# Optimization experiments

Hardware: AMD Instinct MI355X
Metric: run time of the kernel (lower is better)

## Reference

```python
import jax, jax.numpy as jnp
import numpy as np

B, C, H, W = 8, 512, 64, 64
WS, NH = 8, 16
HD = C // NH
SCALE = float(HD) ** -0.5
L = WS * WS  # tokens per window
BN_EPS = 1e-5


def _rel_index():
    # Swin relative position index, (L, L) int table into (2*WS-1)^2 bias rows
    ch = np.arange(WS)
    coords = np.stack(np.meshgrid(ch, ch, indexing='ij'))  # (2, WS, WS)
    cf = coords.reshape(2, -1)
    rel = cf[:, :, None] - cf[:, None, :]
    rel = rel.transpose(1, 2, 0).copy()
    rel[:, :, 0] += WS - 1
    rel[:, :, 1] += WS - 1
    rel[:, :, 0] *= 2 * WS - 1
    return jnp.asarray(rel.sum(-1))

REL_IDX = _rel_index()


def conv2d(x, w, pad=0, groups=1):
    return jax.lax.conv_general_dilated(
        x, w, (1, 1), [(pad, pad), (pad, pad)],
        feature_group_count=groups,
        dimension_numbers=('NCHW', 'OIHW', 'NCHW'))


def bn(x, g, b):
    # eval-mode BatchNorm with running_mean=0, running_var=1 (fresh init)
    inv = 1.0 / np.sqrt(1.0 + BN_EPS)
    return g[None, :, None, None] * (x * inv) + b[None, :, None, None]


def avgpool(x, kh, kw, ph, pw):
    # torch AvgPool2d: zero padding, count_include_pad=True
    s = jax.lax.reduce_window(x, 0.0, jax.lax.add, (1, 1, kh, kw), (1, 1, 1, 1),
                              ((0, 0), (0, 0), (ph, ph), (pw, pw)))
    return s / (kh * kw)


def setup_inputs() -> dict:
    key = jax.random.key(0)
    ks = jax.random.split(key, 8)
    r = lambda k, s: jax.random.normal(k, s, dtype=jnp.float32) * 0.02
    return {
        'x': jax.random.normal(ks[0], (B, C, H, W), dtype=jnp.float32),
        'w_lc1': r(ks[1], (C, C, 1, 1)),
        'g1': jnp.ones((C,), jnp.float32), 'b1': jnp.zeros((C,), jnp.float32),
        'w_lc2': r(ks[2], (C, C, 3, 3)),
        'g2': jnp.ones((C,), jnp.float32), 'b2': jnp.zeros((C,), jnp.float32),
        'w_qkv': r(ks[3], (3 * C, C, 1, 1)),
        'rel_table': r(ks[4], ((2 * WS - 1) * (2 * WS - 1), NH)),
        'w_dw': r(ks[5], (C, 1, WS, WS)),
        'g3': jnp.ones((C,), jnp.float32), 'b3': jnp.zeros((C,), jnp.float32),
        'w_pw': r(ks[6], (C, C, 1, 1)),
    }


def reference(x, w_lc1, g1, b1, w_lc2, g2, b2, w_qkv, rel_table, w_dw, g3, b3, w_pw):
    # local branch: 1x1 conv+BN  +  3x3 conv+BN
    local = bn(conv2d(x, w_lc1), g1, b1) + bn(conv2d(x, w_lc2, pad=1), g2, b2)

    # H, W divisible by WS -> pad() is a no-op; Hp, Wp = H, W
    hh, ww = H // WS, W // WS
    qkv = conv2d(x, w_qkv)  # (B, 3C, H, W)
    # 'b (qkv h d) (hh ws1) (ww ws2) -> qkv (b hh ww) h (ws1 ws2) d'
    qkv = qkv.reshape(B, 3, NH, HD, hh, WS, ww, WS)
    qkv = qkv.transpose(1, 0, 4, 6, 2, 5, 7, 3).reshape(3, B * hh * ww, NH, L, HD)
    q, k, v = qkv[0], qkv[1], qkv[2]

    dots = jnp.einsum('bhid,bhjd->bhij', q, k) * SCALE  # (Bw, NH, L, L)
    bias = rel_table[REL_IDX]                            # (L, L, NH)
    dots = dots + bias.transpose(2, 0, 1)[None]
    attn = jax.nn.softmax(dots, axis=-1)
    out = jnp.einsum('bhij,bhjd->bhid', attn, v)         # (Bw, NH, L, HD)

    # '(b hh ww) h (ws1 ws2) d -> b (h d) (hh ws1) (ww ws2)'
    out = out.reshape(B, hh, ww, NH, WS, WS, HD)
    out = out.transpose(0, 3, 6, 1, 4, 2, 5).reshape(B, C, H, W)

    ax = avgpool(jnp.pad(out, ((0, 0), (0, 0), (0, 1), (0, 0)), mode='reflect'),
                 WS, 1, WS // 2 - 1, 0)
    ay = avgpool(jnp.pad(out, ((0, 0), (0, 0), (0, 0), (0, 1)), mode='reflect'),
                 1, WS, 0, WS // 2 - 1)
    out = ax + ay + local

    # pad_out + SeparableConvBN(kernel=WS): depthwise conv -> BN -> 1x1 conv
    out = jnp.pad(out, ((0, 0), (0, 0), (0, 1), (0, 1)), mode='reflect')
    out = conv2d(out, w_dw, pad=(WS - 1) // 2, groups=C)
    out = bn(out, g3, b3)
    out = conv2d(out, w_pw)
    return out[:, :, :H, :W]
```

## Files before the change

### kernel.cpp

```cpp
#include <hip/hip_runtime.h>

#define INVBN 0.9999950000374997f
#define ATT_SCALE 0.17677669529663687f

typedef short bf16x8 __attribute__((ext_vector_type(8)));
typedef float f32x4  __attribute__((ext_vector_type(4)));
typedef unsigned short us8v __attribute__((ext_vector_type(8)));

#define AS1C(p) ((const __attribute__((address_space(1))) void*)(p))
#define AS3(p)  ((__attribute__((address_space(3))) void*)(p))

#define VMCNT_BARRIER(Nstr) do {                                   \
    asm volatile("s_waitcnt vmcnt(" Nstr ")" ::: "memory");        \
    __builtin_amdgcn_s_barrier(); } while (0)

__device__ __forceinline__ float bf2f(unsigned short u) {
    return __uint_as_float(((unsigned)u) << 16);
}
__device__ __forceinline__ unsigned short f2bf(float f) {
    unsigned u = __float_as_uint(f);
    u += 0x7FFFu + ((u >> 16) & 1u);
    return (unsigned short)(u >> 16);
}

__global__ __launch_bounds__(256)
void repack_kernel(const float* __restrict__ W2, const float* __restrict__ W1,
                   const float* __restrict__ Wq, const float* __restrict__ Wp,
                   const float* __restrict__ g1, const float* __restrict__ g2,
                   const float* __restrict__ b1, const float* __restrict__ b2,
                   const float* __restrict__ RT,
                   unsigned short* __restrict__ Wt, unsigned short* __restrict__ WqO,
                   unsigned short* __restrict__ WpO, float* __restrict__ bsum,
                   float* __restrict__ biasM)
{
    int i = blockIdx.x * 256 + threadIdx.x;
    if (i < 512) bsum[i] = b1[i] + b2[i];
    if (i < 786432) WqO[i] = f2bf(Wq[i]);
    if (i < 262144) WpO[i] = f2bf(Wp[i]);
    if (i < 16384) {
        int h = i >> 10, rem = i & 1023;
        int frag = rem >> 6, lane = rem & 63;
        int fi = frag >> 2, fj = frag & 3;
        int q  = 16 * fj + (lane & 15);
        int kb = 16 * fi + ((lane >> 4) << 2);
        int yi = q >> 3, xi = q & 7;
        float4 o;
        float* op = (float*)&o;
#pragma unroll
        for (int r = 0; r < 4; ++r) {
            int j = kb + r;
            int ridx = (yi - (j >> 3) + 7) * 15 + (xi - (j & 7) + 7);
            op[r] = RT[ridx * 16 + h];
        }
        *(float4*)&biasM[(size_t)i * 4] = o;
    }
    if (i >= 2359296) return;
    int tap = i / 262144;
    int rem = i - tap * 262144;
    int m   = rem >> 9;
    float v = g2[m] * INVBN * W2[(size_t)rem * 9 + tap];
    if (tap == 4) v = fmaf(g1[m] * INVBN, W1[rem], v);
    Wt[i] = f2bf(v);
}

__global__ __launch_bounds__(256)
void pad_transpose_kernel(const float* __restrict__ X, unsigned short* __restrict__ XT)
{
    int ph = blockIdx.x;
    int b  = blockIdx.y;
    int t  = threadIdx.x;
    unsigned short* rowbase = XT + ((size_t)b * 4356 + (size_t)ph * 66) * 512;
    uint4 z = make_uint4(0, 0, 0, 0);
    if (ph == 0 || ph == 65) {
        uint4* p4 = (uint4*)rowbase;
        for (int i = t; i < 4224; i += 256) p4[i] = z;
        return;
    }
    if (t < 64)       ((uint4*)rowbase)[t] = z;
    else if (t < 128) ((uint4*)(rowbase + 65 * 512))[t - 64] = z;

    int h = ph - 1;
    __shared__ float tile[64][65];
    const float* xb = X + (size_t)b * 512 * 4096 + h * 64;
    for (int cc = 0; cc < 8; ++cc) {
        int c0 = cc * 64;
        __syncthreads();
#pragma unroll
        for (int i = 0; i < 4; ++i) {
            int cl = i * 16 + (t >> 4);
            int w0 = (t & 15) * 4;
            *(float4*)&tile[cl][w0] =
                *(const float4*)&xb[(size_t)(c0 + cl) * 4096 + w0];
        }
        __syncthreads();
#pragma unroll
        for (int it = 0; it < 2; ++it) {
            int wl = it * 32 + (t >> 3);
            int cs = (t & 7) * 8;
            us8v v;
#pragma unroll
            for (int e = 0; e < 8; ++e) v[e] = f2bf(tile[cs + e][wl]);
            *(us8v*)&rowbase[(size_t)(1 + wl) * 512 + c0 + cs] = v;
        }
    }
}

template<int NTAPS, bool PAD, typename OT>
__global__ __launch_bounds__(512, 2)
void mfma_gemm256(const unsigned short* __restrict__ A,
                  const unsigned short* __restrict__ Bw,
                  const float* __restrict__ bias,
                  OT* __restrict__ Out, int M)
{
    __shared__ __align__(16) unsigned short ldsbuf[65536];

    const int t    = threadIdx.x;
    const int wid  = t >> 6, lane = t & 63;
    const int wr   = wid >> 2, wc = wid & 3;
    const int lrow = lane & 15, lk = lane >> 4;
    const int n0 = blockIdx.x * 256;
    const int m0 = blockIdx.y * 256;
    const int b  = blockIdx.z;
    const unsigned short* Ab = A + (size_t)b * (PAD ? 4356 * 512 : 4096 * 512);
    OT* Ob = Out + (size_t)b * ((size_t)M * 4096);

    const unsigned short* src[4];
    {
        int rsub = lane >> 2, ch = lane & 3;
        int chs  = ch ^ ((rsub >> 1) & 3);
#pragma unroll
        for (int i = 0; i < 4; ++i) {
            if (wid < 4) {
                int p = n0 + (wid * 4 + i) * 16 + rsub;
                if (PAD) {
                    int h = p >> 6, w = p & 63;
                    src[i] = Ab + (size_t)((h + 1) * 66 + (w + 1)) * 512 + chs * 8;
                } else {
                    src[i] = Ab + (size_t)p * 512 + chs * 8;
                }
            } else {
                int m = m0 + ((wid - 4) * 4 + i) * 16 + rsub;
                src[i] = Bw + (size_t)m * 512 + chs * 8;
            }
        }
    }

    f32x4 acc[8][4] = {};

    const int ck0 = (lk ^ ((lrow >> 1) & 3)) * 8;

    auto aScal = [&](int tt) -> int {
        if (NTAPS == 1) return tt * 32;
        int tap = tt >> 4;
        return (tap / 3 - 1) * (66 * 512) + (tap % 3 - 1) * 512 + (tt & 15) * 32;
    };
    auto bScal = [&](int tt) -> int {
        if (NTAPS == 1) return tt * 32;
        return (tt >> 4) * (M * 512) + (tt & 15) * 32;
    };
    auto STAGE = [&](int bufk, int aoff, int boff) {
        int off = (wid < 4) ? aoff : boff;
#pragma unroll
        for (int i = 0; i < 4; ++i)
            __builtin_amdgcn_global_load_lds(
                AS1C(src[i] + off),
                AS3(&ldsbuf[bufk * 16384 + (wid * 4 + i) * 512]), 16, 0, 0);
    };
    auto COMPUTE = [&](int bufk) {
        const unsigned short* Ak = &ldsbuf[bufk * 16384];
        const unsigned short* Bk = &ldsbuf[bufk * 16384 + 8192];
        bf16x8 af[8], bfr[4];
#pragma unroll
        for (int f = 0; f < 8; ++f)
            af[f] = *(const bf16x8*)&Ak[(wr * 128 + f * 16 + lrow) * 32 + ck0];
#pragma unroll
        for (int g = 0; g < 4; ++g)
            bfr[g] = *(const bf16x8*)&Bk[(wc * 64 + g * 16 + lrow) * 32 + ck0];
        __builtin_amdgcn_s_setprio(1);
#pragma unroll
        for (int f = 0; f < 8; ++f)
#pragma unroll
            for (int g = 0; g < 4; ++g)
                acc[f][g] = __builtin_amdgcn_mfma_f32_16x16x32_bf16(
                    af[f], bfr[g], acc[f][g], 0, 0, 0);
        __builtin_amdgcn_s_setprio(0);
    };

    constexpr int NT = NTAPS * 16;

    STAGE(0, aScal(0), bScal(0));
    STAGE(1, aScal(1), bScal(1));
    STAGE(2, aScal(2), bScal(2));
    VMCNT_BARRIER("8");

#pragma unroll 1
    for (int tb = 0; tb < NT - 4; tb += 4) {
        STAGE(3, aScal(tb + 3), bScal(tb + 3)); COMPUTE(0); VMCNT_BARRIER("8");
        STAGE(0, aScal(tb + 4), bScal(tb + 4)); COMPUTE(1); VMCNT_BARRIER("8");
        STAGE(1, aScal(tb + 5), bScal(tb + 5)); COMPUTE(2); VMCNT_BARRIER("8");
        STAGE(2, aScal(tb + 6), bScal(tb + 6)); COMPUTE(3); VMCNT_BARRIER("8");
    }
    STAGE(3, aScal(NT - 1), bScal(NT - 1)); COMPUTE(0); VMCNT_BARRIER("8");
    COMPUTE(1); VMCNT_BARRIER("4");
    COMPUTE(2); VMCNT_BARRIER("0");
    COMPUTE(3);

#pragma unroll
    for (int g = 0; g < 4; ++g) {
        int m = m0 + wc * 64 + g * 16 + lrow;
        float bv = bias ? bias[m] : 0.f;
        size_t mrow = (size_t)m * 4096;
#pragma unroll
        for (int f = 0; f < 8; ++f) {
            int nb = n0 + wr * 128 + f * 16 + lk * 4;
            f32x4 a4 = acc[f][g];
            if constexpr (sizeof(OT) == 2) {
                ushort4 o;
                o.x = f2bf(a4[0] + bv);
                o.y = f2bf(a4[1] + bv);
                o.z = f2bf(a4[2] + bv);
                o.w = f2bf(a4[3] + bv);
                *(ushort4*)&Ob[mrow + nb] = o;
            } else {
                *(float4*)&Ob[mrow + nb] =
                    make_float4(a4[0] + bv, a4[1] + bv, a4[2] + bv, a4[3] + bv);
            }
        }
    }
}

__global__ __launch_bounds__(256)
void attn_mfma_kernel(const unsigned short* __restrict__ QKV,
                      const float* __restrict__ biasM,
                      unsigned short* __restrict__ OutB)
{
    __shared__ short smem[4 * 9216];
    int t = threadIdx.x;
    int wv = t >> 6, lane = t & 63;
    int wing = blockIdx.x >> 2;
    int head = (blockIdx.x & 3) * 4 + wv;
    int b    = blockIdx.y;
    int hhi = wing >> 3, wwi = wing & 7;
    int sp0 = hhi * 512 + wwi * 8;
    int ch0 = head * 32;
    const unsigned short* Qg = QKV + (size_t)b * 1536 * 4096;

    short* Qtm = smem + wv * 9216;
    short* Ktm = Qtm + 2304;
    short* Pq  = Qtm + 4608;

    {
        int d  = lane & 31;
        int rb = lane >> 5;
#pragma unroll
        for (int i = 0; i < 4; ++i) {
            int r = rb + 2 * i;
            us8v q8 = *(const us8v*)&Qg[(size_t)(ch0 + d) * 4096 + sp0 + r * 64];
            us8v k8 = *(const us8v*)&Qg[(size_t)(512 + ch0 + d) * 4096 + sp0 + r * 64];
#pragma unroll
            for (int e = 0; e < 8; ++e) {
                Qtm[(r * 8 + e) * 36 + d] = (short)q8[e];
                Ktm[(r * 8 + e) * 36 + d] = (short)k8[e];
            }
        }
    }

    int lrow = lane & 15, lk = lane >> 4;

    bf16x8 kf[4], qf[4];
#pragma unroll
    for (int f = 0; f < 4; ++f) {
        kf[f] = *(const bf16x8*)&Ktm[(lrow + 16 * f) * 36 + lk * 8];
        qf[f] = *(const bf16x8*)&Qtm[(lrow + 16 * f) * 36 + lk * 8];
    }
    f32x4 s[4][4] = {};
#pragma unroll
    for (int fi = 0; fi < 4; ++fi)
#pragma unroll
        for (int fj = 0; fj < 4; ++fj)
            s[fi][fj] = __builtin_amdgcn_mfma_f32_16x16x32_bf16(
                kf[fi], qf[fj], s[fi][fj], 0, 0, 0);

    const float* bM = biasM + (size_t)head * 4096;
    float rs[4];
#pragma unroll
    for (int fj = 0; fj < 4; ++fj) {
        float v[4][4];
#pragma unroll
        for (int fi = 0; fi < 4; ++fi) {
            float4 bv = *(const float4*)&bM[((fi * 4 + fj) * 64 + lane) * 4];
            const float* bvp = (const float*)&bv;
#pragma unroll
            for (int r = 0; r < 4; ++r)
                v[fi][r] = fmaf(s[fi][fj][r], ATT_SCALE, bvp[r]);
        }
        float m = -1e30f;
#pragma unroll
        for (int fi = 0; fi < 4; ++fi)
#pragma unroll
            for (int r = 0; r < 4; ++r) m = fmaxf(m, v[fi][r]);
        m = fmaxf(m, __shfl_xor(m, 16));
        m = fmaxf(m, __shfl_xor(m, 32));
        float ev[4][4];
        float sum = 0.f;
#pragma unroll
        for (int fi = 0; fi < 4; ++fi)
#pragma unroll
            for (int r = 0; r < 4; ++r) {
                ev[fi][r] = __expf(v[fi][r] - m);
                sum += ev[fi][r];
            }
        sum += __shfl_xor(sum, 16);
        sum += __shfl_xor(sum, 32);
        rs[fj] = 1.f / sum;
#pragma unroll
        for (int fi = 0; fi < 4; ++fi) {
            unsigned p0 = (unsigned)f2bf(ev[fi][0]) | ((unsigned)f2bf(ev[fi][1]) << 16);
            unsigned p1 = (unsigned)f2bf(ev[fi][2]) | ((unsigned)f2bf(ev[fi][3]) << 16);
            *(uint2*)&Pq[(lrow + 16 * fj) * 72 + 16 * fi + lk * 4] = make_uint2(p0, p1);
        }
    }

    f32x4 o[2][4] = {};
#pragma unroll
    for (int ks = 0; ks < 2; ++ks) {
        bf16x8 vf[2], pf[4];
#pragma unroll
        for (int fid = 0; fid < 2; ++fid)
            vf[fid] = *(const bf16x8*)&Qg[(size_t)(1024 + ch0 + 16 * fid + lrow) * 4096
                                          + sp0 + (lk + 4 * ks) * 64];
#pragma unroll
        for (int fjq = 0; fjq < 4; ++fjq)
            pf[fjq] = *(const bf16x8*)&Pq[(lrow + 16 * fjq) * 72 + ks * 32 + lk * 8];
#pragma unroll
        for (int fid = 0; fid < 2; ++fid)
#pragma unroll
            for (int fjq = 0; fjq < 4; ++fjq)
                o[fid][fjq] = __builtin_amdgcn_mfma_f32_16x16x32_bf16(
                    vf[fid], pf[fjq], o[fid][fjq], 0, 0, 0);
    }

#pragma unroll
    for (int fjq = 0; fjq < 4; ++fjq) {
        int q = lrow + 16 * fjq;
        float rr = rs[fjq];
#pragma unroll
        for (int fid = 0; fid < 2; ++fid) {
            int dch = 16 * fid + lk * 4;
#pragma unroll
            for (int r = 0; r < 4; ++r)
                Pq[(dch + r) * 72 + q] = (short)f2bf(o[fid][fjq][r] * rr);
        }
    }
    unsigned short* Out = OutB + (size_t)b * 512 * 4096;
#pragma unroll
    for (int j = 0; j < 4; ++j) {
        int dch  = lane & 31;
        int tokc = (lane >> 5) + 2 * j;
        us8v vv = *(const us8v*)&Pq[dch * 72 + tokc * 8];
        *(us8v*)&Out[(size_t)(ch0 + dch) * 4096 + sp0 + tokc * 64] = vv;
    }
}

__global__ __launch_bounds__(256)
void pooldw_kernel(const unsigned short* __restrict__ A, const unsigned short* __restrict__ L,
                   const float* __restrict__ Wd,
                   const float* __restrict__ g3, const float* __restrict__ b3,
                   unsigned short* __restrict__ U)
{
    int bc = blockIdx.x;
    int c  = bc & 511;
    __shared__ float pad[72][72];
    int t = threadIdx.x;
    float* pf = &pad[0][0];
#pragma unroll
    for (int i = 0; i < 21; ++i) {
        int e = i * 256 + t;
        if (e < 5184) pf[e] = 0.f;
    }
    __syncthreads();

    const unsigned short* ap = A + (size_t)bc * 4096;
#pragma unroll
    for (int i = 0; i < 4; ++i) {
        int idx = i * 256 + t;
        int y = idx >> 4, x4 = (idx & 15) * 4;
        ushort4 a4 = ((const ushort4*)ap)[idx];
        *(float4*)&pad[3 + y][4 + x4] =
            make_float4(bf2f(a4.x), bf2f(a4.y), bf2f(a4.z), bf2f(a4.w));
    }
    if (t < 64)       pad[67][4 + t] = bf2f(ap[62 * 64 + t]);
    else if (t < 128) { int y = t - 64; pad[3 + y][68] = bf2f(ap[y * 64 + 62]); }
    else if (t == 128) pad[67][68] = bf2f(ap[62 * 64 + 62]);
    __syncthreads();

    const unsigned short* lp = L + (size_t)bc * 4096;
    int u  = t & 7, rr = t >> 3;
    int w0 = u * 8;
    float res[2][8];
#pragma unroll
    for (int g = 0; g < 2; ++g) {
        int h = g * 32 + rr;
        float4 sxlo = make_float4(0.f, 0.f, 0.f, 0.f);
        float4 sxhi = make_float4(0.f, 0.f, 0.f, 0.f);
#pragma unroll
        for (int i = 0; i < 8; ++i) {
            float4 a = *(const float4*)&pad[h + i][4 + w0];
            float4 bq = *(const float4*)&pad[h + i][8 + w0];
            sxlo.x += a.x; sxlo.y += a.y; sxlo.z += a.z; sxlo.w += a.w;
            sxhi.x += bq.x; sxhi.y += bq.y; sxhi.z += bq.z; sxhi.w += bq.w;
        }
        float sx[8] = {sxlo.x, sxlo.y, sxlo.z, sxlo.w, sxhi.x, sxhi.y, sxhi.z, sxhi.w};
        float win[16];
        *(float4*)&win[0]  = *(const float4*)&pad[3 + h][w0];
        *(float4*)&win[4]  = *(const float4*)&pad[3 + h][w0 + 4];
        *(float4*)&win[8]  = *(const float4*)&pad[3 + h][w0 + 8];
        *(float4*)&win[12] = *(const float4*)&pad[3 + h][w0 + 12];
        us8v l8 = *(const us8v*)&lp[h * 64 + w0];
#pragma unroll
        for (int p = 0; p < 8; ++p) {
            float sy = 0.f;
#pragma unroll
            for (int i = 1; i <= 8; ++i) sy += win[p + i];
            res[g][p] = fmaf(0.125f, sx[p] + sy, bf2f((unsigned short)l8[p]));
        }
    }
    __syncthreads();

#pragma unroll
    for (int g = 0; g < 2; ++g) {
        int h = g * 32 + rr;
        *(float4*)&pad[3 + h][4 + w0] = make_float4(res[g][0], res[g][1], res[g][2], res[g][3]);
        *(float4*)&pad[3 + h][8 + w0] = make_float4(res[g][4], res[g][5], res[g][6], res[g][7]);
    }
    __syncthreads();
    if (t < 64)       pad[67][4 + t] = pad[65][4 + t];
    else if (t < 128) { int y = t - 64; pad[3 + y][68] = pad[3 + y][66]; }
    else if (t == 128) pad[67][68] = pad[65][66];
    __syncthreads();

    const float* wdp = Wd + c * 64;
    float gc  = g3[c] * INVBN;
    float bcv = b3[c];
#pragma unroll
    for (int g = 0; g < 2; ++g) {
        int h = g * 32 + rr;
        float acc2[8];
#pragma unroll
        for (int p = 0; p < 8; ++p) acc2[p] = 0.f;
#pragma unroll
        for (int i = 0; i < 8; ++i) {
            float win[16];
            *(float4*)&win[0]  = *(const float4*)&pad[h + i][w0];
            *(float4*)&win[4]  = *(const float4*)&pad[h + i][w0 + 4];
            *(float4*)&win[8]  = *(const float4*)&pad[h + i][w0 + 8];
            *(float4*)&win[12] = *(const float4*)&pad[h + i][w0 + 12];
#pragma unroll
            for (int j = 0; j < 8; ++j) {
                float wv = wdp[i * 8 + j];
#pragma unroll
                for (int p = 0; p < 8; ++p)
                    acc2[p] = fmaf(wv, win[p + 1 + j], acc2[p]);
            }
        }
        us8v o8;
#pragma unroll
        for (int p = 0; p < 8; ++p) o8[p] = (short)f2bf(gc * acc2[p] + bcv);
        *(us8v*)&U[(size_t)bc * 4096 + h * 64 + w0] = o8;
    }
}

__global__ __launch_bounds__(256)
void transpose_cp_kernel(const unsigned short* __restrict__ U, unsigned short* __restrict__ Ut)
{
    int pt = blockIdx.x;
    int b  = blockIdx.y;
    const unsigned short* Ub = U + (size_t)b * 512 * 4096;
    unsigned short* Utb = Ut + (size_t)b * 4096 * 512;
    __shared__ unsigned short tile[64][72];
    int t = threadIdx.x;
    int p0 = pt * 64;

    for (int cc = 0; cc < 8; ++cc) {
        int c0 = cc * 64;
        __syncthreads();
        {
            int cl = t >> 2, px = (t & 3) * 16;
            const unsigned short* src = &Ub[(size_t)(c0 + cl) * 4096 + p0 + px];
            *(us8v*)&tile[cl][px]     = *(const us8v*)src;
            *(us8v*)&tile[cl][px + 8] = *(const us8v*)(src + 8);
        }
        __syncthreads();
        {
            int pl = t >> 2, cx = (t & 3) * 16;
            us8v o0, o1;
#pragma unroll
            for (int e = 0; e < 8; ++e) {
                o0[e] = tile[cx + e][pl];
                o1[e] = tile[cx + 8 + e][pl];
            }
            unsigned short* dst = &Utb[(size_t)(p0 + pl) * 512 + c0 + cx];
            *(us8v*)dst       = o0;
            *(us8v*)(dst + 8) = o1;
        }
    }
}

extern "C" void kernel_launch(void* const* d_in, const int* in_sizes, int n_in,
                              void* d_out, int out_size, void* d_ws, size_t ws_size,
                              hipStream_t stream)
{
    (void)in_sizes; (void)n_in; (void)out_size;
    const float* x     = (const float*)d_in[0];
    const float* w_lc1 = (const float*)d_in[1];
    const float* g1    = (const float*)d_in[2];
    const float* b1    = (const float*)d_in[3];
    const float* w_lc2 = (const float*)d_in[4];
    const float* g2    = (const float*)d_in[5];
    const float* b2    = (const float*)d_in[6];
    const float* w_qkv = (const float*)d_in[7];
    const float* rt    = (const float*)d_in[8];
    const float* w_dw  = (const float*)d_in[9];
    const float* g3    = (const float*)d_in[10];
    const float* b3    = (const float*)d_in[11];
    const float* w_pw  = (const float*)d_in[12];
    float* out = (float*)d_out;

    unsigned short* S        = (unsigned short*)d_ws;
    unsigned short* local_us = S;
    unsigned short* xt_us    = S + 16777216;
    unsigned short* attnO    = xt_us;
    unsigned short* u_us     = xt_us;
    unsigned short* wt3_us   = S + 34619392;
    unsigned short* wq_us    = S + 36978688;
    unsigned short* wpw_us   = S + 37765120;
    float*          bsum     = (float*)(S + 38027264);
    float*          biasM    = (float*)(S + 38028288);
    unsigned short* qkv_us   = S + 38552576;
    unsigned short* ut_us    = local_us;

    const bool full = ws_size >= (size_t)(38552576 + 50331648) * 2;

    repack_kernel<<<dim3(9216), 256, 0, stream>>>(w_lc2, w_lc1, w_qkv, w_pw,
                                                  g1, g2, b1, b2, rt,
                                                  wt3_us, wq_us, wpw_us, bsum, biasM);
    pad_transpose_kernel<<<dim3(66, 8), 256, 0, stream>>>(x, xt_us);
    mfma_gemm256<9, true, unsigned short><<<dim3(16, 2, 8), 512, 0, stream>>>(
        xt_us, wt3_us, bsum, local_us, 512);

    if (full) {
        mfma_gemm256<1, true, unsigned short><<<dim3(16, 6, 8), 512, 0, stream>>>(
            xt_us, wq_us, nullptr, qkv_us, 1536);
        attn_mfma_kernel<<<dim3(256, 8), 256, 0, stream>>>(qkv_us, biasM, attnO);
    } else {
        for (int b = 0; b < 8; ++b) {
            mfma_gemm256<1, true, unsigned short><<<dim3(16, 6, 1), 512, 0, stream>>>(
                xt_us + (size_t)b * 4356 * 512, wq_us, nullptr, qkv_us, 1536);
            attn_mfma_kernel<<<dim3(256, 1), 256, 0, stream>>>(
                qkv_us, biasM, attnO + (size_t)b * 2097152);
        }
    }

    pooldw_kernel<<<dim3(4096), 256, 0, stream>>>(attnO, local_us, w_dw, g3, b3, u_us);
    transpose_cp_kernel<<<dim3(64, 8), 256, 0, stream>>>(u_us, ut_us);
    mfma_gemm256<1, false, float><<<dim3(16, 2, 8), 512, 0, stream>>>(
        ut_us, wpw_us, nullptr, out, 512);
}
```

Baseline: 466.3 us.

## Fuse QKV projection GEMM into window attention kernel

Replaces the separate QKV GEMM and attention kernels with one kernel. Each block stages a window's 64 tokens of transposed input into LDS, and each wave computes its head's Q, K and V with MFMA, reading weights directly from global memory. The bf16 QKV intermediate no longer makes a round trip through HBM, and the per-batch fallback path is removed. In exchange, the 64x512 input tile is re-loaded by each of the four head-group blocks per window, and unblocked weight reads from global may have poor reuse.

```diff
diff --git a/kernel.cpp b/kernel.cpp
--- a/kernel.cpp
+++ b/kernel.cpp
@@ -146,7 +146,6 @@
     }
 
     f32x4 acc[8][4] = {};
-
     const int ck0 = (lk ^ ((lrow >> 1) & 3)) * 8;
 
     auto aScal = [&](int tt) -> int {
@@ -230,42 +229,80 @@
 }
 
 __global__ __launch_bounds__(256)
-void attn_mfma_kernel(const unsigned short* __restrict__ QKV,
-                      const float* __restrict__ biasM,
-                      unsigned short* __restrict__ OutB)
-{
-    __shared__ short smem[4 * 9216];
+void fused_qkv_attn_kernel(const unsigned short* __restrict__ XT,
+                           const unsigned short* __restrict__ W,
+                           const float* __restrict__ biasM,
+                           unsigned short* __restrict__ OutB)
+{
+    __shared__ __align__(16) unsigned short xts[32768];
+    __shared__ short pws[4][6912];
+
     int t = threadIdx.x;
-    int wv = t >> 6, lane = t & 63;
-    int wing = blockIdx.x >> 2;
-    int head = (blockIdx.x & 3) * 4 + wv;
-    int b    = blockIdx.y;
+    int wid = t >> 6, lane = t & 63;
+    int wing = blockIdx.y, b = blockIdx.z;
+    int head = blockIdx.x * 4 + wid;
     int hhi = wing >> 3, wwi = wing & 7;
     int sp0 = hhi * 512 + wwi * 8;
     int ch0 = head * 32;
-    const unsigned short* Qg = QKV + (size_t)b * 1536 * 4096;
-
-    short* Qtm = smem + wv * 9216;
+    const unsigned short* xtb = XT + (size_t)b * (4356 * 512);
+
+#pragma unroll
+    for (int rd = 0; rd < 16; ++rd) {
+        int tk  = rd * 4 + wid;
+        int rr  = tk >> 3, cdx = tk & 7;
+        int grow = (hhi * 8 + rr + 1) * 66 + (wwi * 8 + cdx + 1);
+        int cs  = lane ^ (tk & 7);
+        __builtin_amdgcn_global_load_lds(
+            AS1C(xtb + (size_t)grow * 512 + cs * 8),
+            AS3(&xts[tk * 512 + lane * 8]), 16, 0, 0);
+    }
+    asm volatile("s_waitcnt vmcnt(0)" ::: "memory");
+    __builtin_amdgcn_s_barrier();
+
+    int lrow = lane & 15, lk = lane >> 4;
+    short* Qtm = pws[wid];
     short* Ktm = Qtm + 2304;
-    short* Pq  = Qtm + 4608;
-
-    {
-        int d  = lane & 31;
-        int rb = lane >> 5;
-#pragma unroll
-        for (int i = 0; i < 4; ++i) {
-            int r = rb + 2 * i;
-            us8v q8 = *(const us8v*)&Qg[(size_t)(ch0 + d) * 4096 + sp0 + r * 64];
-            us8v k8 = *(const us8v*)&Qg[(size_t)(512 + ch0 + d) * 4096 + sp0 + r * 64];
-#pragma unroll
-            for (int e = 0; e < 8; ++e) {
-                Qtm[(r * 8 + e) * 36 + d] = (short)q8[e];
-                Ktm[(r * 8 + e) * 36 + d] = (short)k8[e];
+    short* Vtm = Qtm + 4608;
+    short* Pq  = Qtm;
+
+#pragma unroll 1
+    for (int mtx = 0; mtx < 3; ++mtx) {
+        const unsigned short* wbase = W + (size_t)(mtx * 512 + ch0) * 512;
+        f32x4 aq[4][2] = {};
+#pragma unroll
+        for (int ks = 0; ks < 16; ++ks) {
+            bf16x8 b0 = *(const bf16x8*)&wbase[(size_t)lrow * 512 + ks * 32 + lk * 8];
+            bf16x8 b1 = *(const bf16x8*)&wbase[(size_t)(16 + lrow) * 512 + ks * 32 + lk * 8];
+#pragma unroll
+            for (int tf = 0; tf < 4; ++tf) {
+                int row = tf * 16 + lrow;
+                int cc  = (ks * 4 + lk) ^ (row & 7);
+                bf16x8 af = *(const bf16x8*)&xts[row * 512 + cc * 8];
+                aq[tf][0] = __builtin_amdgcn_mfma_f32_16x16x32_bf16(af, b0, aq[tf][0], 0, 0, 0);
+                aq[tf][1] = __builtin_amdgcn_mfma_f32_16x16x32_bf16(af, b1, aq[tf][1], 0, 0, 0);
             }
         }
-    }
-
-    int lrow = lane & 15, lk = lane >> 4;
+        if (mtx < 2) {
+            short* dst = (mtx == 0) ? Qtm : Ktm;
+#pragma unroll
+            for (int tf = 0; tf < 4; ++tf)
+#pragma unroll
+                for (int cf = 0; cf < 2; ++cf)
+#pragma unroll
+                    for (int r = 0; r < 4; ++r)
+                        dst[(16 * tf + lk * 4 + r) * 36 + 16 * cf + lrow] =
+                            (short)f2bf(aq[tf][cf][r]);
+        } else {
+#pragma unroll
+            for (int tf = 0; tf < 4; ++tf)
+#pragma unroll
+                for (int cf = 0; cf < 2; ++cf)
+#pragma unroll
+                    for (int r = 0; r < 4; ++r)
+                        Vtm[(16 * cf + lrow) * 72 + 16 * tf + lk * 4 + r] =
+                            (short)f2bf(aq[tf][cf][r]);
+        }
+    }
 
     bf16x8 kf[4], qf[4];
 #pragma unroll
@@ -327,8 +364,7 @@
         bf16x8 vf[2], pf[4];
 #pragma unroll
         for (int fid = 0; fid < 2; ++fid)
-            vf[fid] = *(const bf16x8*)&Qg[(size_t)(1024 + ch0 + 16 * fid + lrow) * 4096
-                                          + sp0 + (lk + 4 * ks) * 64];
+            vf[fid] = *(const bf16x8*)&Vtm[(16 * fid + lrow) * 72 + (lk + 4 * ks) * 8];
 #pragma unroll
         for (int fjq = 0; fjq < 4; ++fjq)
             pf[fjq] = *(const bf16x8*)&Pq[(lrow + 16 * fjq) * 72 + ks * 32 + lk * 8];
@@ -510,7 +546,7 @@
                               void* d_out, int out_size, void* d_ws, size_t ws_size,
                               hipStream_t stream)
 {
-    (void)in_sizes; (void)n_in; (void)out_size;
+    (void)in_sizes; (void)n_in; (void)out_size; (void)ws_size;
     const float* x     = (const float*)d_in[0];
     const float* w_lc1 = (const float*)d_in[1];
     const float* g1    = (const float*)d_in[2];
@@ -529,17 +565,14 @@
     unsigned short* S        = (unsigned short*)d_ws;
     unsigned short* local_us = S;
     unsigned short* xt_us    = S + 16777216;
-    unsigned short* attnO    = xt_us;
-    unsigned short* u_us     = xt_us;
     unsigned short* wt3_us   = S + 34619392;
     unsigned short* wq_us    = S + 36978688;
     unsigned short* wpw_us   = S + 37765120;
     float*          bsum     = (float*)(S + 38027264);
     float*          biasM    = (float*)(S + 38028288);
-    unsigned short* qkv_us   = S + 38552576;
+    unsigned short* attnO    = S + 38552576;
+    unsigned short* u_us     = attnO;
     unsigned short* ut_us    = local_us;
-
-    const bool full = ws_size >= (size_t)(38552576 + 50331648) * 2;
 
     repack_kernel<<<dim3(9216), 256, 0, stream>>>(w_lc2, w_lc1, w_qkv, w_pw,
                                                   g1, g2, b1, b2, rt,
@@ -547,20 +580,8 @@
     pad_transpose_kernel<<<dim3(66, 8), 256, 0, stream>>>(x, xt_us);
     mfma_gemm256<9, true, unsigned short><<<dim3(16, 2, 8), 512, 0, stream>>>(
         xt_us, wt3_us, bsum, local_us, 512);
-
-    if (full) {
-        mfma_gemm256<1, true, unsigned short><<<dim3(16, 6, 8), 512, 0, stream>>>(
-            xt_us, wq_us, nullptr, qkv_us, 1536);
-        attn_mfma_kernel<<<dim3(256, 8), 256, 0, stream>>>(qkv_us, biasM, attnO);
-    } else {
-        for (int b = 0; b < 8; ++b) {
-            mfma_gemm256<1, true, unsigned short><<<dim3(16, 6, 1), 512, 0, stream>>>(
-                xt_us + (size_t)b * 4356 * 512, wq_us, nullptr, qkv_us, 1536);
-            attn_mfma_kernel<<<dim3(256, 1), 256, 0, stream>>>(
-                qkv_us, biasM, attnO + (size_t)b * 2097152);
-        }
-    }
-
+    fused_qkv_attn_kernel<<<dim3(4, 64, 8), 256, 0, stream>>>(
+        xt_us, wq_us, biasM, attnO);
     pooldw_kernel<<<dim3(4096), 256, 0, stream>>>(attnO, local_us, w_dw, g3, b3, u_us);
     transpose_cp_kernel<<<dim3(64, 8), 256, 0, stream>>>(u_us, ut_us);
     mfma_gemm256<1, false, float><<<dim3(16, 2, 8), 512, 0, stream>>>(
```

New measurement: 516.9 us. +10.8%, slower.

## Switch GEMM pipeline to double-buffered BK=64 stages with one block per CU

Applied to the files above, without the earlier changes.

Replaces the 4-stage BK=32 global_load_lds ring with a 2-stage BK=64 double buffer, using an 8-chunk XOR swizzle in LDS and two k-substeps per compute. Launch bounds drop to one 512-thread block per CU. The aim is to halve the number of barriers per K and give each wave more MFMA work per stage. The cost is shallower prefetch, an extra barrier after each compute, and less latency hiding from a second resident block.

```diff
diff --git a/kernel.cpp b/kernel.cpp
--- a/kernel.cpp
+++ b/kernel.cpp
@@ -9,10 +9,6 @@
 
 #define AS1C(p) ((const __attribute__((address_space(1))) void*)(p))
 #define AS3(p)  ((__attribute__((address_space(3))) void*)(p))
-
-#define VMCNT_BARRIER(Nstr) do {                                   \
-    asm volatile("s_waitcnt vmcnt(" Nstr ")" ::: "memory");        \
-    __builtin_amdgcn_s_barrier(); } while (0)
 
 __device__ __forceinline__ float bf2f(unsigned short u) {
     return __uint_as_float(((unsigned)u) << 16);
@@ -106,7 +102,7 @@
 }
 
 template<int NTAPS, bool PAD, typename OT>
-__global__ __launch_bounds__(512, 2)
+__global__ __launch_bounds__(512, 1)
 void mfma_gemm256(const unsigned short* __restrict__ A,
                   const unsigned short* __restrict__ Bw,
                   const float* __restrict__ bias,
@@ -124,14 +120,15 @@
     const unsigned short* Ab = A + (size_t)b * (PAD ? 4356 * 512 : 4096 * 512);
     OT* Ob = Out + (size_t)b * ((size_t)M * 4096);
 
-    const unsigned short* src[4];
+    const unsigned short* src[8];
     {
-        int rsub = lane >> 2, ch = lane & 3;
-        int chs  = ch ^ ((rsub >> 1) & 3);
-#pragma unroll
-        for (int i = 0; i < 4; ++i) {
+        int rsub = lane >> 3, ch = lane & 7;
+        int chs  = ch ^ rsub;
+#pragma unroll
+        for (int i = 0; i < 8; ++i) {
+            int row = (wid & 3) * 64 + i * 8 + rsub;
             if (wid < 4) {
-                int p = n0 + (wid * 4 + i) * 16 + rsub;
+                int p = n0 + row;
                 if (PAD) {
                     int h = p >> 6, w = p & 63;
                     src[i] = Ab + (size_t)((h + 1) * 66 + (w + 1)) * 512 + chs * 8;
@@ -139,71 +136,70 @@
                     src[i] = Ab + (size_t)p * 512 + chs * 8;
                 }
             } else {
-                int m = m0 + ((wid - 4) * 4 + i) * 16 + rsub;
-                src[i] = Bw + (size_t)m * 512 + chs * 8;
+                src[i] = Bw + (size_t)(m0 + row) * 512 + chs * 8;
             }
         }
     }
+    const int dbase = (wid >> 2) * 16384 + (wid & 3) * 4096;
 
     f32x4 acc[8][4] = {};
 
-    const int ck0 = (lk ^ ((lrow >> 1) & 3)) * 8;
-
     auto aScal = [&](int tt) -> int {
-        if (NTAPS == 1) return tt * 32;
-        int tap = tt >> 4;
-        return (tap / 3 - 1) * (66 * 512) + (tap % 3 - 1) * 512 + (tt & 15) * 32;
+        if (NTAPS == 1) return tt * 64;
+        int tap = tt >> 3;
+        return (tap / 3 - 1) * (66 * 512) + (tap % 3 - 1) * 512 + (tt & 7) * 64;
     };
     auto bScal = [&](int tt) -> int {
-        if (NTAPS == 1) return tt * 32;
-        return (tt >> 4) * (M * 512) + (tt & 15) * 32;
+        if (NTAPS == 1) return tt * 64;
+        return (tt >> 3) * (M * 512) + (tt & 7) * 64;
     };
     auto STAGE = [&](int bufk, int aoff, int boff) {
         int off = (wid < 4) ? aoff : boff;
 #pragma unroll
-        for (int i = 0; i < 4; ++i)
+        for (int i = 0; i < 8; ++i)
             __builtin_amdgcn_global_load_lds(
                 AS1C(src[i] + off),
-                AS3(&ldsbuf[bufk * 16384 + (wid * 4 + i) * 512]), 16, 0, 0);
+                AS3(&ldsbuf[bufk * 32768 + dbase + i * 512]), 16, 0, 0);
     };
     auto COMPUTE = [&](int bufk) {
-        const unsigned short* Ak = &ldsbuf[bufk * 16384];
-        const unsigned short* Bk = &ldsbuf[bufk * 16384 + 8192];
-        bf16x8 af[8], bfr[4];
-#pragma unroll
-        for (int f = 0; f < 8; ++f)
-            af[f] = *(const bf16x8*)&Ak[(wr * 128 + f * 16 + lrow) * 32 + ck0];
-#pragma unroll
-        for (int g = 0; g < 4; ++g)
-            bfr[g] = *(const bf16x8*)&Bk[(wc * 64 + g * 16 + lrow) * 32 + ck0];
+        const unsigned short* Ak = &ldsbuf[bufk * 32768];
+        const unsigned short* Bk = &ldsbuf[bufk * 32768 + 16384];
         __builtin_amdgcn_s_setprio(1);
 #pragma unroll
-        for (int f = 0; f < 8; ++f)
+        for (int kk = 0; kk < 2; ++kk) {
+            const int ck = ((kk * 4 + lk) ^ (lrow & 7)) * 8;
+            bf16x8 af[8], bfr[4];
+#pragma unroll
+            for (int f = 0; f < 8; ++f)
+                af[f] = *(const bf16x8*)&Ak[(wr * 128 + f * 16 + lrow) * 64 + ck];
 #pragma unroll
             for (int g = 0; g < 4; ++g)
-                acc[f][g] = __builtin_amdgcn_mfma_f32_16x16x32_bf16(
-                    af[f], bfr[g], acc[f][g], 0, 0, 0);
+                bfr[g] = *(const bf16x8*)&Bk[(wc * 64 + g * 16 + lrow) * 64 + ck];
+#pragma unroll
+            for (int f = 0; f < 8; ++f)
+#pragma unroll
+                for (int g = 0; g < 4; ++g)
+                    acc[f][g] = __builtin_amdgcn_mfma_f32_16x16x32_bf16(
+                        af[f], bfr[g], acc[f][g], 0, 0, 0);
+        }
         __builtin_amdgcn_s_setprio(0);
     };
 
-    constexpr int NT = NTAPS * 16;
+    constexpr int NT = (NTAPS == 1) ? 8 : 72;
 
     STAGE(0, aScal(0), bScal(0));
-    STAGE(1, aScal(1), bScal(1));
-    STAGE(2, aScal(2), bScal(2));
-    VMCNT_BARRIER("8");
-
 #pragma unroll 1
-    for (int tb = 0; tb < NT - 4; tb += 4) {
-        STAGE(3, aScal(tb + 3), bScal(tb + 3)); COMPUTE(0); VMCNT_BARRIER("8");
-        STAGE(0, aScal(tb + 4), bScal(tb + 4)); COMPUTE(1); VMCNT_BARRIER("8");
-        STAGE(1, aScal(tb + 5), bScal(tb + 5)); COMPUTE(2); VMCNT_BARRIER("8");
-        STAGE(2, aScal(tb + 6), bScal(tb + 6)); COMPUTE(3); VMCNT_BARRIER("8");
-    }
-    STAGE(3, aScal(NT - 1), bScal(NT - 1)); COMPUTE(0); VMCNT_BARRIER("8");
-    COMPUTE(1); VMCNT_BARRIER("4");
-    COMPUTE(2); VMCNT_BARRIER("0");
-    COMPUTE(3);
+    for (int tt = 0; tt < NT; ++tt) {
+        if (tt + 1 < NT) {
+            STAGE((tt + 1) & 1, aScal(tt + 1), bScal(tt + 1));
+            asm volatile("s_waitcnt vmcnt(8)" ::: "memory");
+        } else {
+            asm volatile("s_waitcnt vmcnt(0)" ::: "memory");
+        }
+        __builtin_amdgcn_s_barrier();
+        COMPUTE(tt & 1);
+        __builtin_amdgcn_s_barrier();
+    }
 
 #pragma unroll
     for (int g = 0; g < 4; ++g) {
```

After: 455.9 us. -2.2%, faster.
